# Kernel tuning notes

Measured on AMD Instinct MI355X. Metric: run time of the kernel, lower is better.

Reference implementation:

```python
import jax, jax.numpy as jnp
import numpy as np
from jax import lax

DILS = (1, 2, 4, 8)
POOLS = (1, 2, 3, 6)
EPS = 1e-3  # Keras BatchNormalization default epsilon


def conv2d(x, w, b, dil=1):
    y = lax.conv_general_dilated(x, w, window_strides=(1, 1), padding='SAME',
                                 rhs_dilation=(dil, dil),
                                 dimension_numbers=('NHWC', 'HWIO', 'NHWC'))
    return y + b


def bn(x, g, be, m, v):
    return (x - m) * (g * lax.rsqrt(v + EPS)) + be


def avg_pool_same(x, ps):
    if ps == 1:
        return x
    win = (1, ps, ps, 1)
    s = lax.reduce_window(x, 0.0, lax.add, win, win, 'SAME')
    c = lax.reduce_window(jnp.ones(x.shape[:3] + (1,), x.dtype), 0.0, lax.add, win, win, 'SAME')
    return s / c  # TF avg-pool SAME excludes padded zeros from the count


def setup_inputs() -> dict:
    key = jax.random.key(0)
    ks = iter(jax.random.split(key, 40))
    f = 64  # filters
    cin = 64
    d = {}
    d['x'] = jax.random.normal(next(ks), (2, 64, 64, cin), jnp.float32)
    nb = len(DILS)
    d['conv_w'] = jax.random.normal(next(ks), (nb, 3, 3, cin, f)) * 0.05
    d['conv_b'] = jax.random.normal(next(ks), (nb, f)) * 0.05
    d['bn_g'] = jnp.ones((nb, f)) + jax.random.normal(next(ks), (nb, f)) * 0.05
    d['bn_b'] = jax.random.normal(next(ks), (nb, f)) * 0.05
    d['bn_m'] = jax.random.normal(next(ks), (nb, f)) * 0.05
    d['bn_v'] = jax.random.uniform(next(ks), (nb, f), minval=0.5, maxval=1.5)
    dk = f // 8
    d['q_w'] = jax.random.normal(next(ks), (nb, 1, 1, f, dk)) * 0.05
    d['q_b'] = jax.random.normal(next(ks), (nb, dk)) * 0.05
    d['k_w'] = jax.random.normal(next(ks), (nb, 1, 1, f, dk)) * 0.05
    d['k_b'] = jax.random.normal(next(ks), (nb, dk)) * 0.05
    d['v_w'] = jax.random.normal(next(ks), (nb, 1, 1, f, f)) * 0.05
    d['v_b'] = jax.random.normal(next(ks), (nb, f)) * 0.05
    d['attn_gamma'] = jax.random.normal(next(ks), (nb,)) * 0.1
    cat = f * nb  # 256, input channels to pyramid convs
    npool = len(POOLS)
    fq = f // 4  # 16
    d['ppl_w'] = jax.random.normal(next(ks), (npool, 1, 1, cat, fq)) * 0.05
    d['ppl_b'] = jax.random.normal(next(ks), (npool, fq)) * 0.05
    d['ppl_bn_g'] = jnp.ones((npool, fq)) + jax.random.normal(next(ks), (npool, fq)) * 0.05
    d['ppl_bn_b'] = jax.random.normal(next(ks), (npool, fq)) * 0.05
    d['ppl_bn_m'] = jax.random.normal(next(ks), (npool, fq)) * 0.05
    d['ppl_bn_v'] = jax.random.uniform(next(ks), (npool, fq), minval=0.5, maxval=1.5)
    cfused = cat + npool * fq  # 320
    d['proj_w'] = jax.random.normal(next(ks), (1, 1, cfused, f)) * 0.05
    d['proj_b'] = jax.random.normal(next(ks), (f,)) * 0.05
    d['pbn_g'] = jnp.ones((f,)) + jax.random.normal(next(ks), (f,)) * 0.05
    d['pbn_b'] = jax.random.normal(next(ks), (f,)) * 0.05
    d['pbn_m'] = jax.random.normal(next(ks), (f,)) * 0.05
    d['pbn_v'] = jax.random.uniform(next(ks), (f,), minval=0.5, maxval=1.5)
    return d


def reference(x, conv_w, conv_b, bn_g, bn_b, bn_m, bn_v,
              q_w, q_b, k_w, k_b, v_w, v_b, attn_gamma,
              ppl_w, ppl_b, ppl_bn_g, ppl_bn_b, ppl_bn_m, ppl_bn_v,
              proj_w, proj_b, pbn_g, pbn_b, pbn_m, pbn_v):
    B, H, W, _ = x.shape
    branches = []
    for i, dil in enumerate(DILS):
        # dilated conv -> BN (inference) -> ReLU
        b = jax.nn.relu(bn(conv2d(x, conv_w[i], conv_b[i], dil),
                           bn_g[i], bn_b[i], bn_m[i], bn_v[i]))
        C = b.shape[-1]
        # full spatial self-attention over HW tokens
        q = conv2d(b, q_w[i], q_b[i]).reshape(B, H * W, -1)  # [B, HW, C/8]
        k = conv2d(b, k_w[i], k_b[i]).reshape(B, H * W, -1)
        v = conv2d(b, v_w[i], v_b[i]).reshape(B, H * W, C)
        attn = jax.nn.softmax(jnp.einsum('bnd,bmd->bnm', q, k), axis=-1)  # [B, HW, HW]
        o = jnp.einsum('bnm,bmc->bnc', attn, v).reshape(B, H, W, C)
        branches.append(attn_gamma[i] * o + b)
    fused = jnp.concatenate(branches, axis=-1)  # [B, H, W, 256]
    pooled = [fused]
    for j, ps in enumerate(POOLS):
        p = avg_pool_same(fused, ps)
        p = bn(conv2d(p, ppl_w[j], ppl_b[j]),
               ppl_bn_g[j], ppl_bn_b[j], ppl_bn_m[j], ppl_bn_v[j])
        p = jax.image.resize(p, (B, H, W, p.shape[-1]), method='bilinear')
        pooled.append(p)
    fused = jnp.concatenate(pooled, axis=-1)  # [B, H, W, 320]
    out = jax.nn.relu(bn(conv2d(fused, proj_w, proj_b), pbn_g, pbn_b, pbn_m, pbn_v))
    return out
```

## Files before the change

kernel.cpp:

```cpp
#include <hip/hip_runtime.h>
#include <hip/hip_bf16.h>
#include <stdint.h>

typedef unsigned short u16;
typedef short bs8 __attribute__((ext_vector_type(8)));
typedef unsigned short u16x4 __attribute__((ext_vector_type(4)));
typedef float vf4 __attribute__((ext_vector_type(4)));
typedef float vf16 __attribute__((ext_vector_type(16)));

__device__ __forceinline__ u16 f2bf(float f) {
    uint32_t u = __builtin_bit_cast(uint32_t, f);
    uint32_t r = u + 0x7FFFu + ((u >> 16) & 1u);
    return (u16)(r >> 16);
}
__device__ __forceinline__ float bf2f(u16 v) {
    return __builtin_bit_cast(float, (uint32_t)v << 16);
}

#define EPSBN 1e-3f
#define L2E 1.4426950408889634f

__global__ __launch_bounds__(256) void prep_k(
    const float* __restrict__ x, const float* __restrict__ cw,
    const float* __restrict__ qw, const float* __restrict__ kw,
    const float* __restrict__ vw, const float* __restrict__ pjw,
    u16* __restrict__ xbf, u16* __restrict__ wpk,
    u16* __restrict__ wqk_pk, u16* __restrict__ wv_pk, u16* __restrict__ wfin_pk)
{
    if (blockIdx.x < 512) {
        int t = blockIdx.x * 256 + threadIdx.x;
        int idx = t * 4;
        vf4 v = *(const vf4*)(x + idx);
        u16x4 o = { f2bf(v[0]), f2bf(v[1]), f2bf(v[2]), f2bf(v[3]) };
        *(u16x4*)(xbf + idx) = o;
    } else if (blockIdx.x < 1088) {
        int t2 = (blockIdx.x - 512) * 256 + threadIdx.x;
        if (t2 < 147456) {
            int cout = t2 & 63, rest = t2 >> 6;
            int cin = rest & 63, itap = rest >> 6;
            wpk[(((size_t)itap * 8 + (cin >> 3)) * 64 + cout) * 8 + (cin & 7)] = f2bf(cw[t2]);
        }
    } else if (blockIdx.x < 1168) {
        int t3 = (blockIdx.x - 1088) * 256 + threadIdx.x;
        if (t3 < 4096) {
            int j = t3 & 7, l = (t3 >> 3) & 63, kk = (t3 >> 9) & 1, i = t3 >> 10;
            int cin = kk * 32 + ((l >> 4) << 3) + j, row = l & 15;
            float val = (row < 8) ? qw[((size_t)(i * 64 + cin)) * 8 + row] * L2E
                                  : kw[((size_t)(i * 64 + cin)) * 8 + row - 8];
            wqk_pk[t3] = f2bf(val);
        } else {
            int e = t3 - 4096;
            int j = e & 7, l = (e >> 3) & 63, kk = (e >> 9) & 1;
            int ct = (e >> 10) & 3, i = e >> 12;
            int cin = kk * 32 + ((l >> 4) << 3) + j, cout = ct * 16 + (l & 15);
            wv_pk[e] = f2bf(vw[((size_t)(i * 64 + cin)) * 64 + cout]);
        }
    } else {
        int t4 = (blockIdx.x - 1168) * 256 + threadIdx.x;
        if (t4 < 20480) {
            int e = t4;
            int j = e & 7; e >>= 3;
            int rcol = e & 15; e >>= 4;
            int ct = e & 3; e >>= 2;
            int g = e & 3; int kc = e >> 2;
            int cin = kc * 32 + g * 8 + j, co = ct * 16 + rcol;
            wfin_pk[t4] = f2bf(pjw[(size_t)cin * 64 + co]);
        }
    }
}

__global__ __launch_bounds__(256) void conv_mfma_k(
    const u16* __restrict__ xbf, const u16* __restrict__ wpk,
    const float* __restrict__ cb, const float* __restrict__ bng,
    const float* __restrict__ bnb, const float* __restrict__ bnm,
    const float* __restrict__ bnv, const u16* __restrict__ wqk_pk,
    const u16* __restrict__ wv_pk, const float* __restrict__ qb,
    const float* __restrict__ kb, const float* __restrict__ vb,
    u16* __restrict__ b_bf, u16* __restrict__ qbuf,
    u16* __restrict__ kbuf, u16* __restrict__ vT)
{
    __shared__ u16 blds[32][72];
    const int ib = blockIdx.x & 7, pixtile = blockIdx.x >> 3;
    const int i = ib >> 1, b = ib & 1, dil = 1 << i;
    const int wave = __builtin_amdgcn_readfirstlane(threadIdx.x >> 6);
    const int lane = threadIdx.x & 63;
    const int g = lane >> 4, r = lane & 15;
    const int pixsub = wave & 1, ch = wave >> 1;
    const int pixbase = pixtile * 32 + pixsub * 16;
    const int h = pixbase >> 6, w0 = pixbase & 63;

    vf4 acc0 = {0.f, 0.f, 0.f, 0.f}, acc1 = {0.f, 0.f, 0.f, 0.f};

    for (int ky = 0; ky < 3; ++ky) {
        int hy = h + (ky - 1) * dil;
        if (hy < 0 || hy >= 64) continue;
        const u16* xrow = xbf + (size_t)((b * 64 + hy) * 64) * 64;
        for (int kx = 0; kx < 3; ++kx) {
            int wx = w0 + r + (kx - 1) * dil;
            bool valid = (wx >= 0) && (wx < 64);
            const u16* ap = xrow + (valid ? wx : 0) * 64 + g * 8;
            int tap = ky * 3 + kx;
            const u16* wb = wpk + (size_t)((i * 9 + tap) * 8) * 512;
#pragma unroll
            for (int c2 = 0; c2 < 2; ++c2) {
                bs8 av = {};
                if (valid) av = *(const bs8*)(ap + c2 * 32);
                const u16* bp = wb + (size_t)(c2 * 4 + g) * 512 + (ch * 32 + r) * 8;
                bs8 bv0 = *(const bs8*)(bp);
                bs8 bv1 = *(const bs8*)(bp + 16 * 8);
                acc0 = __builtin_amdgcn_mfma_f32_16x16x32_bf16(av, bv0, acc0, 0, 0, 0);
                acc1 = __builtin_amdgcn_mfma_f32_16x16x32_bf16(av, bv1, acc1, 0, 0, 0);
            }
        }
    }
#pragma unroll
    for (int ct = 0; ct < 2; ++ct) {
        int cidx = ch * 32 + ct * 16 + r;
        int cgl = i * 64 + cidx;
        float sc = bng[cgl] * rsqrtf(bnv[cgl] + EPSBN);
        float sh = (cb[cgl] - bnm[cgl]) * sc + bnb[cgl];
        vf4 a = ct ? acc1 : acc0;
#pragma unroll
        for (int rr = 0; rr < 4; ++rr) {
            float y = fmaxf(a[rr] * sc + sh, 0.f);
            u16 yb = f2bf(y);
            b_bf[((size_t)ib * 4096 + pixbase + g * 4 + rr) * 64 + cidx] = yb;
            blds[pixsub * 16 + g * 4 + rr][cidx] = yb;
        }
    }
    __syncthreads();

    const int ps2 = wave & 1, role = wave >> 1;
    const int n0 = pixtile * 32 + ps2 * 16;
    bs8 xb0 = *(const bs8*)(&blds[ps2 * 16 + r][g * 8]);
    bs8 xb1 = *(const bs8*)(&blds[ps2 * 16 + r][32 + g * 8]);

    if (role == 1) {
        const u16* wq = wqk_pk + (size_t)i * 1024 + lane * 8;
        bs8 wq0 = *(const bs8*)(wq);
        bs8 wq1 = *(const bs8*)(wq + 512);
        vf4 s = (vf4){0.f, 0.f, 0.f, 0.f};
        s = __builtin_amdgcn_mfma_f32_16x16x32_bf16(wq0, xb0, s, 0, 0, 0);
        s = __builtin_amdgcn_mfma_f32_16x16x32_bf16(wq1, xb1, s, 0, 0, 0);
        if (g < 2) {
            int d0 = g * 4;
            u16x4 o;
#pragma unroll
            for (int reg = 0; reg < 4; ++reg)
                o[reg] = f2bf(s[reg] + qb[i * 8 + d0 + reg] * L2E);
            *(u16x4*)(qbuf + ((size_t)ib * 4096 + n0 + r) * 8 + d0) = o;
        } else {
            int d0 = (g - 2) * 4;
            u16x4 o;
#pragma unroll
            for (int reg = 0; reg < 4; ++reg)
                o[reg] = f2bf(s[reg] + kb[i * 8 + d0 + reg]);
            *(u16x4*)(kbuf + ((size_t)ib * 4096 + n0 + r) * 8 + d0) = o;
        }
    }
#pragma unroll
    for (int c2t = 0; c2t < 2; ++c2t) {
        int ct = role * 2 + c2t;
        const u16* wv = wv_pk + ((size_t)i * 4 + ct) * 1024 + lane * 8;
        bs8 wv0 = *(const bs8*)(wv);
        bs8 wv1 = *(const bs8*)(wv + 512);
        vf4 a = (vf4){0.f, 0.f, 0.f, 0.f};
        a = __builtin_amdgcn_mfma_f32_16x16x32_bf16(wv0, xb0, a, 0, 0, 0);
        a = __builtin_amdgcn_mfma_f32_16x16x32_bf16(wv1, xb1, a, 0, 0, 0);
#pragma unroll
        for (int reg = 0; reg < 4; ++reg) {
            int row = ct * 16 + g * 4 + reg;
            vT[((size_t)ib * 64 + row) * 4096 + n0 + r] = f2bf(a[reg] + vb[i * 64 + row]);
        }
    }
}

__global__ __launch_bounds__(256) void attn_k(
    const u16* __restrict__ qbuf, const u16* __restrict__ kbuf,
    const u16* __restrict__ vT, u16* __restrict__ pacc,
    float* __restrict__ ppsum)
{
    __shared__ __align__(16) char smem[36864];
    u16* klds = (u16*)(smem + 32768);

    const int bid = blockIdx.x;
    const int ib = bid & 7, ks = (bid >> 3) & 7, qblk = bid >> 6;
    const int yb = ks * 8 + ib;
    const int wave = __builtin_amdgcn_readfirstlane(threadIdx.x >> 6);
    const int lane = threadIdx.x & 63;
    const int ql = lane & 31;
    const int hb = lane >> 5;
    const int q0 = qblk * 256 + wave * 64;
    const int tid = threadIdx.x;

    const int kb_tbl[8] = {0, 8, 4, 12, 16, 24, 20, 28};
    const int kperm = (ql & 3) + kb_tbl[ql >> 2];

    bs8 qfa = {}, qfb = {};
    if (hb == 0) {
        qfa = *(const bs8*)(qbuf + ((size_t)ib * 4096 + q0 + ql) * 8);
        qfb = *(const bs8*)(qbuf + ((size_t)ib * 4096 + q0 + 32 + ql) * 8);
    }

    vf16 a0a, a1a, a0b, a1b;
#pragma unroll
    for (int r = 0; r < 16; ++r) { a0a[r] = 0.f; a1a[r] = 0.f; a0b[r] = 0.f; a1b[r] = 0.f; }
    float psa = 0.f, psb = 0.f;

    const u16* vsrc = vT + (size_t)ib * 64 * 4096;
    const u16* ksrc = kbuf + (size_t)ib * 4096 * 8;
    const int sc_ = tid >> 2, sp_ = tid & 3;
    const char* ldsb = (const char*)smem;

    for (int kblk = ks * 2; kblk < ks * 2 + 2; ++kblk) {
        const int kb = kblk * 256;
        __syncthreads();
        {
            const u16* vrow = vsrc + (size_t)sc_ * 4096 + kb;
            char* ldsw = (char*)smem;
#pragma unroll
            for (int s = 0; s < 8; ++s) {
                int key = sp_ * 8 + s * 32;
                bs8 val = *(const bs8*)(vrow + key);
                int lin = sc_ * 512 + key * 2;
                *(bs8*)(ldsw + (lin ^ ((sc_ & 7) << 4))) = val;
            }
            bs8 kvv = *(const bs8*)(ksrc + (size_t)(kb + tid) * 8);
            *(bs8*)(klds + tid * 8) = kvv;
        }
        __syncthreads();

#pragma unroll 2
        for (int ck = 0; ck < 8; ++ck) {
            const int keyb = ck * 32;
            bs8 kA = {};
            if (hb == 0) kA = *(const bs8*)(klds + (keyb + kperm) * 8);
            vf16 z;
#pragma unroll
            for (int r = 0; r < 16; ++r) z[r] = 0.f;
            __builtin_amdgcn_s_setprio(1);
            vf16 Sa = __builtin_amdgcn_mfma_f32_32x32x16_bf16(kA, qfa, z, 0, 0, 0);
            vf16 Sb = __builtin_amdgcn_mfma_f32_32x32x16_bf16(kA, qfb, z, 0, 0, 0);
            __builtin_amdgcn_s_setprio(0);

            const int c0 = ql, c1 = 32 + ql;
            int lin00 = c0 * 512 + (keyb + hb * 8) * 2;
            int lin10 = c1 * 512 + (keyb + hb * 8) * 2;
            bs8 vA00 = *(const bs8*)(ldsb + (lin00 ^ ((c0 & 7) << 4)));
            bs8 vA01 = *(const bs8*)(ldsb + ((lin00 + 32) ^ ((c0 & 7) << 4)));
            bs8 vA10 = *(const bs8*)(ldsb + (lin10 ^ ((c1 & 7) << 4)));
            bs8 vA11 = *(const bs8*)(ldsb + ((lin10 + 32) ^ ((c1 & 7) << 4)));

            {
                float e[16];
#pragma unroll
                for (int r = 0; r < 16; ++r) {
                    e[r] = __builtin_amdgcn_exp2f(Sa[r]);
                    psa += e[r];
                }
                union { uint32_t u[4]; bs8 v; } p0, p1;
#pragma unroll
                for (int j = 0; j < 4; ++j) {
                    uint32_t w0, w1;
                    asm("v_cvt_pk_bf16_f32 %0, %1, %2" : "=v"(w0) : "v"(e[2 * j]), "v"(e[2 * j + 1]));
                    asm("v_cvt_pk_bf16_f32 %0, %1, %2" : "=v"(w1) : "v"(e[8 + 2 * j]), "v"(e[8 + 2 * j + 1]));
                    p0.u[j] = w0;
                    p1.u[j] = w1;
                }
                __builtin_amdgcn_s_setprio(1);
                a0a = __builtin_amdgcn_mfma_f32_32x32x16_bf16(vA00, p0.v, a0a, 0, 0, 0);
                a0a = __builtin_amdgcn_mfma_f32_32x32x16_bf16(vA01, p1.v, a0a, 0, 0, 0);
                a1a = __builtin_amdgcn_mfma_f32_32x32x16_bf16(vA10, p0.v, a1a, 0, 0, 0);
                a1a = __builtin_amdgcn_mfma_f32_32x32x16_bf16(vA11, p1.v, a1a, 0, 0, 0);
                __builtin_amdgcn_s_setprio(0);
            }
            {
                float e[16];
#pragma unroll
                for (int r = 0; r < 16; ++r) {
                    e[r] = __builtin_amdgcn_exp2f(Sb[r]);
                    psb += e[r];
                }
                union { uint32_t u[4]; bs8 v; } p0, p1;
#pragma unroll
                for (int j = 0; j < 4; ++j) {
                    uint32_t w0, w1;
                    asm("v_cvt_pk_bf16_f32 %0, %1, %2" : "=v"(w0) : "v"(e[2 * j]), "v"(e[2 * j + 1]));
                    asm("v_cvt_pk_bf16_f32 %0, %1, %2" : "=v"(w1) : "v"(e[8 + 2 * j]), "v"(e[8 + 2 * j + 1]));
                    p0.u[j] = w0;
                    p1.u[j] = w1;
                }
                __builtin_amdgcn_s_setprio(1);
                a0b = __builtin_amdgcn_mfma_f32_32x32x16_bf16(vA00, p0.v, a0b, 0, 0, 0);
                a0b = __builtin_amdgcn_mfma_f32_32x32x16_bf16(vA01, p1.v, a0b, 0, 0, 0);
                a1b = __builtin_amdgcn_mfma_f32_32x32x16_bf16(vA10, p0.v, a1b, 0, 0, 0);
                a1b = __builtin_amdgcn_mfma_f32_32x32x16_bf16(vA11, p1.v, a1b, 0, 0, 0);
                __builtin_amdgcn_s_setprio(0);
            }
        }
    }

    psa += __shfl_xor(psa, 32);
    psb += __shfl_xor(psb, 32);

    __syncthreads();
    float* tw = (float*)smem + wave * 32 * 67;
#pragma unroll
    for (int t = 0; t < 2; ++t) {
        const int q0t = q0 + t * 32;
#pragma unroll
        for (int ct = 0; ct < 2; ++ct) {
            vf16 a = t ? (ct ? a1b : a0b) : (ct ? a1a : a0a);
#pragma unroll
            for (int r = 0; r < 16; ++r) {
                int c = ct * 32 + (r & 3) + 8 * (r >> 2) + 4 * hb;
                tw[ql * 67 + c] = a[r];
            }
        }
        u16* pdst = pacc + ((size_t)yb * 4096 + q0t) * 64;
        for (int qq = 0; qq < 32; ++qq)
            pdst[(size_t)qq * 64 + lane] = f2bf(tw[qq * 67 + lane]);
        if (hb == 0)
            ppsum[(size_t)yb * 4096 + q0t + ql] = t ? psb : psa;
    }
}

__global__ __launch_bounds__(256) void combine_k(
    const u16* __restrict__ pacc, const float* __restrict__ ppsum,
    const u16* __restrict__ b_bf, const float* __restrict__ gamma,
    u16* __restrict__ fusedbf)
{
    const int ib = blockIdx.x & 7, qb = blockIdx.x >> 3;
    const int i = ib >> 1, b = ib & 1;
    const int q = qb * 8 + (threadIdx.x >> 5);
    const int c2 = (threadIdx.x & 31) * 2;
    const size_t stride = (size_t)8 * 4096 * 64;
    size_t base = ((size_t)ib * 4096 + q) * 64 + c2;
    float lo = 0.f, hi = 0.f, ps = 0.f;
#pragma unroll
    for (int s = 0; s < 8; ++s) {
        uint32_t u = *(const uint32_t*)(pacc + base + s * stride);
        lo += bf2f((u16)(u & 0xffff));
        hi += bf2f((u16)(u >> 16));
        ps += ppsum[(size_t)(s * 8 + ib) * 4096 + q];
    }
    float rs = gamma[i] / ps;
    uint32_t bv = *(const uint32_t*)(b_bf + base);
    float o0 = rs * lo + bf2f((u16)(bv & 0xffff));
    float o1 = rs * hi + bf2f((u16)(bv >> 16));
    uint32_t ou = ((uint32_t)f2bf(o1) << 16) | f2bf(o0);
    *(uint32_t*)(fusedbf + ((size_t)b * 4096 + q) * 256 + i * 64 + c2) = ou;
}

__global__ __launch_bounds__(256) void pconv_k(
    const u16* __restrict__ fusedbf,
    const float* __restrict__ pw, const float* __restrict__ pbias,
    const float* __restrict__ pg, const float* __restrict__ pbe,
    const float* __restrict__ pm, const float* __restrict__ pv,
    float* __restrict__ po0, float* __restrict__ po1,
    float* __restrict__ po2, float* __restrict__ po3)
{
    __shared__ float plds[16][257];
    const int j = blockIdx.z, b = blockIdx.y;
    const int npix = (j == 0) ? 4096 : (j == 1) ? 1024 : (j == 2) ? 484 : 121;
    if (blockIdx.x * 16 >= npix) return;
    const int co = threadIdx.x & 15;
    const int pixl = threadIdx.x >> 4;
    const int pix = blockIdx.x * 16 + pixl;
    const float* wp = pw + (size_t)j * 256 * 16 + co;
    float acc = pbias[j * 16 + co];

    if (j == 0) {
        const u16* ip = fusedbf + ((size_t)b * 4096 + pix) * 256;
        for (int c8 = 0; c8 < 32; ++c8) {
            bs8 xv = *(const bs8*)(ip + c8 * 8);
#pragma unroll
            for (int e = 0; e < 8; ++e)
                acc = fmaf(bf2f((u16)xv[e]), wp[(c8 * 8 + e) * 16], acc);
        }
    } else {
        const int ps = (j == 1) ? 2 : (j == 2) ? 3 : 6;
        const int od = (j == 1) ? 32 : (j == 2) ? 22 : 11;
        if (pix < npix) {
            const int oh = pix / od, ow = pix % od;
            const int pad = (od * ps - 64) >> 1;
            int hs = oh * ps - pad, wss = ow * ps - pad;
            int h0 = max(hs, 0), h1 = min(hs + ps, 64);
            int w0 = max(wss, 0), w1 = min(wss + ps, 64);
            float s[16];
#pragma unroll
            for (int e = 0; e < 16; ++e) s[e] = 0.f;
            for (int hh = h0; hh < h1; ++hh)
                for (int ww = w0; ww < w1; ++ww) {
                    const u16* p = fusedbf + (((size_t)b * 4096) + hh * 64 + ww) * 256 + co * 16;
                    bs8 v0 = *(const bs8*)(p);
                    bs8 v1 = *(const bs8*)(p + 8);
#pragma unroll
                    for (int e = 0; e < 8; ++e) {
                        s[e] += bf2f((u16)v0[e]);
                        s[8 + e] += bf2f((u16)v1[e]);
                    }
                }
            float inv = 1.f / (float)((h1 - h0) * (w1 - w0));
#pragma unroll
            for (int e = 0; e < 16; ++e) plds[pixl][co * 16 + e] = s[e] * inv;
        }
        __syncthreads();
        if (pix < npix)
            for (int c = 0; c < 256; ++c)
                acc = fmaf(plds[pixl][c], wp[c * 16], acc);
    }
    if (pix < npix) {
        acc = (acc - pm[j * 16 + co]) * (pg[j * 16 + co] * rsqrtf(pv[j * 16 + co] + EPSBN)) + pbe[j * 16 + co];
        float* outp = (j == 0) ? po0 : (j == 1) ? po1 : (j == 2) ? po2 : po3;
        outp[((size_t)b * npix + pix) * 16 + co] = acc;
    }
}

__global__ __launch_bounds__(64) void final_gemm_k(
    const u16* __restrict__ fusedbf, const float* __restrict__ po0,
    const float* __restrict__ po1, const float* __restrict__ po2,
    const float* __restrict__ po3, const u16* __restrict__ wfin_pk,
    const float* __restrict__ pjb, const float* __restrict__ g,
    const float* __restrict__ be, const float* __restrict__ m,
    const float* __restrict__ v, float* __restrict__ out)
{
    const int gpix0 = blockIdx.x * 16;
    const int lane = threadIdx.x & 63;
    const int gg = lane >> 4, r = lane & 15;

    const int p = gpix0 + r;
    const int b = p >> 12, hw = p & 4095, h = hw >> 6, w = hw & 63;
    bs8 pav[2];
#pragma unroll
    for (int t = 0; t < 2; ++t) {
        int jj = t * 2 + (gg >> 1);
        int cc0 = (gg & 1) * 8;
        const float* P = (jj == 0) ? po0 : (jj == 1) ? po1 : (jj == 2) ? po2 : po3;
        int od = (jj == 0) ? 64 : (jj == 1) ? 32 : (jj == 2) ? 22 : 11;
        float scale = (float)od / 64.f;
        float fy = (h + 0.5f) * scale - 0.5f;
        int y0 = (int)floorf(fy);
        float ay = fy - (float)y0;
        int y1 = min(y0 + 1, od - 1);
        y0 = max(y0, 0);
        float fx = (w + 0.5f) * scale - 0.5f;
        int x0 = (int)floorf(fx);
        float ax = fx - (float)x0;
        int x1 = min(x0 + 1, od - 1);
        x0 = max(x0, 0);
        const float* B0 = P + (size_t)b * od * od * 16 + cc0;
        const float* p00 = B0 + (size_t)(y0 * od + x0) * 16;
        const float* p01 = B0 + (size_t)(y0 * od + x1) * 16;
        const float* p10 = B0 + (size_t)(y1 * od + x0) * 16;
        const float* p11 = B0 + (size_t)(y1 * od + x1) * 16;
        union { u16 s[8]; bs8 v8; } o;
#pragma unroll
        for (int cc = 0; cc < 8; ++cc) {
            float top = p00[cc] + ax * (p01[cc] - p00[cc]);
            float bot = p10[cc] + ax * (p11[cc] - p10[cc]);
            o.s[cc] = f2bf(top + ay * (bot - top));
        }
        pav[t] = o.v8;
    }

    vf4 acc[4];
#pragma unroll
    for (int ct = 0; ct < 4; ++ct) acc[ct] = (vf4){0.f, 0.f, 0.f, 0.f};

    const u16* fa = fusedbf + (size_t)p * 256 + gg * 8;
#pragma unroll
    for (int kc = 0; kc < 10; ++kc) {
        bs8 av = (kc < 8) ? *(const bs8*)(fa + kc * 32) : pav[kc - 8];
        const u16* wb = wfin_pk + (size_t)((kc * 4 + gg) * 4) * 128 + r * 8;
#pragma unroll
        for (int ct = 0; ct < 4; ++ct) {
            bs8 bv = *(const bs8*)(wb + ct * 128);
            acc[ct] = __builtin_amdgcn_mfma_f32_16x16x32_bf16(av, bv, acc[ct], 0, 0, 0);
        }
    }
#pragma unroll
    for (int ct = 0; ct < 4; ++ct) {
        int c = ct * 16 + r;
        float sc = g[c] * rsqrtf(v[c] + EPSBN);
        float sh = (pjb[c] - m[c]) * sc + be[c];
#pragma unroll
        for (int reg = 0; reg < 4; ++reg) {
            int pix = gpix0 + gg * 4 + reg;
            out[(size_t)pix * 64 + c] = fmaxf(acc[ct][reg] * sc + sh, 0.f);
        }
    }
}

extern "C" void kernel_launch(void* const* d_in, const int* in_sizes, int n_in,
                              void* d_out, int out_size, void* d_ws, size_t ws_size,
                              hipStream_t stream)
{
    const float* x      = (const float*)d_in[0];
    const float* conv_w = (const float*)d_in[1];
    const float* conv_b = (const float*)d_in[2];
    const float* bn_g   = (const float*)d_in[3];
    const float* bn_b   = (const float*)d_in[4];
    const float* bn_m   = (const float*)d_in[5];
    const float* bn_v   = (const float*)d_in[6];
    const float* q_w    = (const float*)d_in[7];
    const float* q_b    = (const float*)d_in[8];
    const float* k_w    = (const float*)d_in[9];
    const float* k_b    = (const float*)d_in[10];
    const float* v_w    = (const float*)d_in[11];
    const float* v_b    = (const float*)d_in[12];
    const float* gamma  = (const float*)d_in[13];
    const float* ppl_w  = (const float*)d_in[14];
    const float* ppl_b  = (const float*)d_in[15];
    const float* ppl_g  = (const float*)d_in[16];
    const float* ppl_be = (const float*)d_in[17];
    const float* ppl_m  = (const float*)d_in[18];
    const float* ppl_v  = (const float*)d_in[19];
    const float* proj_w = (const float*)d_in[20];
    const float* proj_b = (const float*)d_in[21];
    const float* pbn_g  = (const float*)d_in[22];
    const float* pbn_b  = (const float*)d_in[23];
    const float* pbn_m  = (const float*)d_in[24];
    const float* pbn_v  = (const float*)d_in[25];

    char* ws = (char*)d_ws;
    u16*  xbf     = (u16*)(ws + 0);
    u16*  wpk     = (u16*)(ws + 1048576);
    u16*  wqk_pk  = (u16*)(ws + 1343488);
    u16*  wv_pk   = (u16*)(ws + 1351680);
    u16*  wfin_pk = (u16*)(ws + 1384448);
    u16*  b_bf    = (u16*)(ws + 1425408);
    u16*  qbuf    = (u16*)(ws + 5619712);
    u16*  kbuf    = (u16*)(ws + 6144000);
    u16*  vT      = (u16*)(ws + 6668288);
    u16*  fusedbf = (u16*)(ws + 10862592);
    float* ppsum  = (float*)(ws + 15056896);
    u16*  pacc    = (u16*)(ws + 16105472);
    float* po0    = (float*)(ws + 18917376);
    float* po1    = (float*)(ws + 19441664);
    float* po2    = (float*)(ws + 19572736);
    float* po3    = (float*)(ws + 19634688);
    float* out    = (float*)d_out;

    prep_k<<<dim3(1248), 256, 0, stream>>>(
        x, conv_w, q_w, k_w, v_w, proj_w, xbf, wpk, wqk_pk, wv_pk, wfin_pk);
    conv_mfma_k<<<dim3(1024), 256, 0, stream>>>(
        xbf, wpk, conv_b, bn_g, bn_b, bn_m, bn_v,
        wqk_pk, wv_pk, q_b, k_b, v_b, b_bf, qbuf, kbuf, vT);
    attn_k<<<dim3(1024), 256, 0, stream>>>(qbuf, kbuf, vT, pacc, ppsum);
    combine_k<<<dim3(4096), 256, 0, stream>>>(pacc, ppsum, b_bf, gamma, fusedbf);
    pconv_k<<<dim3(256, 2, 4), 256, 0, stream>>>(
        fusedbf, ppl_w, ppl_b, ppl_g, ppl_be, ppl_m, ppl_v,
        po0, po1, po2, po3);
    final_gemm_k<<<dim3(512), 64, 0, stream>>>(
        fusedbf, po0, po1, po2, po3, wfin_pk, proj_b, pbn_g, pbn_b, pbn_m, pbn_v, out);
}
```

Before: 100.9 us.

## Halve attention key splits, compute row sums via MFMA, write partials in fragment layout

Reduces the attention key-split factor from 8 to 4, so each block processes four key tiles and the grid drops to 512 blocks, halving the partial output traffic and the combine reads. Row sums of exp scores are now computed with an extra MFMA against a ones vector instead of scalar adds. The LDS transpose epilogue is removed: accumulators are written directly in the MFMA fragment layout as packed bf16, and combine_k decodes that layout. This cuts epilogue LDS work and partial-buffer size, but adds MFMA work, leaves fewer blocks to fill the GPU, and uses a less coalesced read pattern in combine.

```diff
diff --git a/kernel.cpp b/kernel.cpp
--- a/kernel.cpp
+++ b/kernel.cpp
@@ -175,16 +175,16 @@
     }
 }
 
-__global__ __launch_bounds__(256) void attn_k(
+__global__ __launch_bounds__(256, 4) void attn_k(
     const u16* __restrict__ qbuf, const u16* __restrict__ kbuf,
-    const u16* __restrict__ vT, u16* __restrict__ pacc,
+    const u16* __restrict__ vT, uint32_t* __restrict__ pacc32,
     float* __restrict__ ppsum)
 {
     __shared__ __align__(16) char smem[36864];
     u16* klds = (u16*)(smem + 32768);
 
     const int bid = blockIdx.x;
-    const int ib = bid & 7, ks = (bid >> 3) & 7, qblk = bid >> 6;
+    const int ib = bid & 7, ks = (bid >> 3) & 3, qblk = bid >> 5;
     const int yb = ks * 8 + ib;
     const int wave = __builtin_amdgcn_readfirstlane(threadIdx.x >> 6);
     const int lane = threadIdx.x & 63;
@@ -201,18 +201,23 @@
         qfa = *(const bs8*)(qbuf + ((size_t)ib * 4096 + q0 + ql) * 8);
         qfb = *(const bs8*)(qbuf + ((size_t)ib * 4096 + q0 + 32 + ql) * 8);
     }
-
-    vf16 a0a, a1a, a0b, a1b;
-#pragma unroll
-    for (int r = 0; r < 16; ++r) { a0a[r] = 0.f; a1a[r] = 0.f; a0b[r] = 0.f; a1b[r] = 0.f; }
-    float psa = 0.f, psb = 0.f;
+    bs8 ones;
+#pragma unroll
+    for (int j = 0; j < 8; ++j) ones[j] = (short)0x3F80;
+
+    vf16 a0a, a1a, a0b, a1b, sa, sb;
+#pragma unroll
+    for (int r = 0; r < 16; ++r) {
+        a0a[r] = 0.f; a1a[r] = 0.f; a0b[r] = 0.f; a1b[r] = 0.f;
+        sa[r] = 0.f; sb[r] = 0.f;
+    }
 
     const u16* vsrc = vT + (size_t)ib * 64 * 4096;
     const u16* ksrc = kbuf + (size_t)ib * 4096 * 8;
     const int sc_ = tid >> 2, sp_ = tid & 3;
     const char* ldsb = (const char*)smem;
 
-    for (int kblk = ks * 2; kblk < ks * 2 + 2; ++kblk) {
+    for (int kblk = ks * 4; kblk < ks * 4 + 4; ++kblk) {
         const int kb = kblk * 256;
         __syncthreads();
         {
@@ -254,10 +259,7 @@
             {
                 float e[16];
 #pragma unroll
-                for (int r = 0; r < 16; ++r) {
-                    e[r] = __builtin_amdgcn_exp2f(Sa[r]);
-                    psa += e[r];
-                }
+                for (int r = 0; r < 16; ++r) e[r] = __builtin_amdgcn_exp2f(Sa[r]);
                 union { uint32_t u[4]; bs8 v; } p0, p1;
 #pragma unroll
                 for (int j = 0; j < 4; ++j) {
@@ -268,6 +270,8 @@
                     p1.u[j] = w1;
                 }
                 __builtin_amdgcn_s_setprio(1);
+                sa = __builtin_amdgcn_mfma_f32_32x32x16_bf16(ones, p0.v, sa, 0, 0, 0);
+                sa = __builtin_amdgcn_mfma_f32_32x32x16_bf16(ones, p1.v, sa, 0, 0, 0);
                 a0a = __builtin_amdgcn_mfma_f32_32x32x16_bf16(vA00, p0.v, a0a, 0, 0, 0);
                 a0a = __builtin_amdgcn_mfma_f32_32x32x16_bf16(vA01, p1.v, a0a, 0, 0, 0);
                 a1a = __builtin_amdgcn_mfma_f32_32x32x16_bf16(vA10, p0.v, a1a, 0, 0, 0);
@@ -277,10 +281,7 @@
             {
                 float e[16];
 #pragma unroll
-                for (int r = 0; r < 16; ++r) {
-                    e[r] = __builtin_amdgcn_exp2f(Sb[r]);
-                    psb += e[r];
-                }
+                for (int r = 0; r < 16; ++r) e[r] = __builtin_amdgcn_exp2f(Sb[r]);
                 union { uint32_t u[4]; bs8 v; } p0, p1;
 #pragma unroll
                 for (int j = 0; j < 4; ++j) {
@@ -291,6 +292,8 @@
                     p1.u[j] = w1;
                 }
                 __builtin_amdgcn_s_setprio(1);
+                sb = __builtin_amdgcn_mfma_f32_32x32x16_bf16(ones, p0.v, sb, 0, 0, 0);
+                sb = __builtin_amdgcn_mfma_f32_32x32x16_bf16(ones, p1.v, sb, 0, 0, 0);
                 a0b = __builtin_amdgcn_mfma_f32_32x32x16_bf16(vA00, p0.v, a0b, 0, 0, 0);
                 a0b = __builtin_amdgcn_mfma_f32_32x32x16_bf16(vA01, p1.v, a0b, 0, 0, 0);
                 a1b = __builtin_amdgcn_mfma_f32_32x32x16_bf16(vA10, p0.v, a1b, 0, 0, 0);
@@ -300,33 +303,29 @@
         }
     }
 
-    psa += __shfl_xor(psa, 32);
-    psb += __shfl_xor(psb, 32);
-
-    __syncthreads();
-    float* tw = (float*)smem + wave * 32 * 67;
 #pragma unroll
     for (int t = 0; t < 2; ++t) {
-        const int q0t = q0 + t * 32;
+        const int qt = (q0 >> 5) + t;
+        vf16 s_ = t ? sb : sa;
 #pragma unroll
         for (int ct = 0; ct < 2; ++ct) {
             vf16 a = t ? (ct ? a1b : a0b) : (ct ? a1a : a0a);
-#pragma unroll
-            for (int r = 0; r < 16; ++r) {
-                int c = ct * 32 + (r & 3) + 8 * (r >> 2) + 4 * hb;
-                tw[ql * 67 + c] = a[r];
+            uint32_t* pdst = pacc32 + ((((size_t)yb * 128 + qt) * 2 + ct) * 512)
+                           + (hb * 32 + ql) * 8;
+#pragma unroll
+            for (int j = 0; j < 8; ++j) {
+                uint32_t w;
+                asm("v_cvt_pk_bf16_f32 %0, %1, %2" : "=v"(w) : "v"(a[2 * j]), "v"(a[2 * j + 1]));
+                pdst[j] = w;
             }
         }
-        u16* pdst = pacc + ((size_t)yb * 4096 + q0t) * 64;
-        for (int qq = 0; qq < 32; ++qq)
-            pdst[(size_t)qq * 64 + lane] = f2bf(tw[qq * 67 + lane]);
         if (hb == 0)
-            ppsum[(size_t)yb * 4096 + q0t + ql] = t ? psb : psa;
+            ppsum[(size_t)yb * 4096 + qt * 32 + ql] = s_[0];
     }
 }
 
 __global__ __launch_bounds__(256) void combine_k(
-    const u16* __restrict__ pacc, const float* __restrict__ ppsum,
+    const uint32_t* __restrict__ pacc32, const float* __restrict__ ppsum,
     const u16* __restrict__ b_bf, const float* __restrict__ gamma,
     u16* __restrict__ fusedbf)
 {
@@ -334,17 +333,23 @@
     const int i = ib >> 1, b = ib & 1;
     const int q = qb * 8 + (threadIdx.x >> 5);
     const int c2 = (threadIdx.x & 31) * 2;
-    const size_t stride = (size_t)8 * 4096 * 64;
-    size_t base = ((size_t)ib * 4096 + q) * 64 + c2;
+    const int qt = q >> 5, ql = q & 31, ct = c2 >> 5, c5 = c2 & 31;
+    const int hb = (c5 >> 2) & 1;
+    const int jw = ((c5 & 2) >> 1) | ((c5 >> 3) << 1);
+    const size_t widx = (((size_t)qt * 2 + ct) * 512) + (hb * 32 + ql) * 8 + jw;
+    const size_t ybstride = (size_t)8 * 128 * 2 * 512;
     float lo = 0.f, hi = 0.f, ps = 0.f;
 #pragma unroll
-    for (int s = 0; s < 8; ++s) {
-        uint32_t u = *(const uint32_t*)(pacc + base + s * stride);
+    for (int s = 0; s < 4; ++s) {
+        int yb = s * 8 + ib;
+        uint32_t u = pacc32[(size_t)yb * (128 * 2 * 512) + widx];
         lo += bf2f((u16)(u & 0xffff));
         hi += bf2f((u16)(u >> 16));
-        ps += ppsum[(size_t)(s * 8 + ib) * 4096 + q];
-    }
+        ps += ppsum[(size_t)yb * 4096 + q];
+    }
+    (void)ybstride;
     float rs = gamma[i] / ps;
+    size_t base = ((size_t)ib * 4096 + q) * 64 + c2;
     uint32_t bv = *(const uint32_t*)(b_bf + base);
     float o0 = rs * lo + bf2f((u16)(bv & 0xffff));
     float o1 = rs * hi + bf2f((u16)(bv >> 16));
@@ -535,7 +540,7 @@
     u16*  vT      = (u16*)(ws + 6668288);
     u16*  fusedbf = (u16*)(ws + 10862592);
     float* ppsum  = (float*)(ws + 15056896);
-    u16*  pacc    = (u16*)(ws + 16105472);
+    uint32_t* pacc32 = (uint32_t*)(ws + 15581184);
     float* po0    = (float*)(ws + 18917376);
     float* po1    = (float*)(ws + 19441664);
     float* po2    = (float*)(ws + 19572736);
@@ -547,8 +552,8 @@
     conv_mfma_k<<<dim3(1024), 256, 0, stream>>>(
         xbf, wpk, conv_b, bn_g, bn_b, bn_m, bn_v,
         wqk_pk, wv_pk, q_b, k_b, v_b, b_bf, qbuf, kbuf, vT);
-    attn_k<<<dim3(1024), 256, 0, stream>>>(qbuf, kbuf, vT, pacc, ppsum);
-    combine_k<<<dim3(4096), 256, 0, stream>>>(pacc, ppsum, b_bf, gamma, fusedbf);
+    attn_k<<<dim3(512), 256, 0, stream>>>(qbuf, kbuf, vT, pacc32, ppsum);
+    combine_k<<<dim3(4096), 256, 0, stream>>>(pacc32, ppsum, b_bf, gamma, fusedbf);
     pconv_k<<<dim3(256, 2, 4), 256, 0, stream>>>(
         fusedbf, ppl_w, ppl_b, ppl_g, ppl_be, ppl_m, ppl_v,
         po0, po1, po2, po3);
```

Result: slower. 243.0 us (+140.9%).
